# Performance work log

Hardware: AMD Instinct MI355X
Metric: run time of the kernel (lower is better)

Reference implementation:

```python
import jax, jax.numpy as jnp
import numpy as np
import math

N, LQ, DIM = 4, 1000, 256
HEADS, DHEAD, DEPTH = 8, 32, 2
LVLS, NPTS, MLP = 5, 4, 512
SCALE = DHEAD ** -0.5
SHAPES = np.array([[128, 128], [64, 64], [32, 32], [16, 16], [8, 8]], np.int32)
AREAS = SHAPES[:, 0] * SHAPES[:, 1]
STARTS = np.concatenate([[0], np.cumsum(AREAS)[:-1]]).astype(np.int32)
LIN = int(AREAS.sum())


def _ln(x, g, b):
    m = jnp.mean(x, -1, keepdims=True)
    v = jnp.var(x, -1, keepdims=True)
    return (x - m) * jax.lax.rsqrt(v + 1e-5) * g + b


def _gelu(x):  # tanh-approx GELU exactly as the torch module
    c = math.sqrt(2.0 / math.pi)
    return 0.5 * x * (1.0 + jnp.tanh(c * (x + 0.044715 * x ** 3)))


def _ms_deform(value, shapes, starts, loc, aw):
    # value [N,Lin,H,D]; loc [N,Lq,H,L,P,2] normalized to [0,1]; aw [N,Lq,H,L,P]
    n, lq, h, L, p, _ = loc.shape
    d = value.shape[-1]
    ni = jnp.arange(n)[:, None, None, None]
    hi = jnp.arange(h)[None, None, :, None]
    out = jnp.zeros((n, lq, h, d), value.dtype)
    for l in range(L):  # fixed small pyramid depth
        Hl, Wl = int(shapes[l, 0]), int(shapes[l, 1])
        s = int(starts[l])
        v = value[:, s:s + Hl * Wl].reshape(n, Hl, Wl, h, d)
        gx = loc[:, :, :, l, :, 0] * Wl - 0.5  # [N,Lq,H,P]
        gy = loc[:, :, :, l, :, 1] * Hl - 0.5
        x0 = jnp.floor(gx); y0 = jnp.floor(gy)
        lx = gx - x0; ly = gy - y0
        x0i = x0.astype(jnp.int32); y0i = y0.astype(jnp.int32)
        def corner(yi, xi):
            ok = ((yi >= 0) & (yi < Hl) & (xi >= 0) & (xi < Wl)).astype(value.dtype)
            g = v[ni, jnp.clip(yi, 0, Hl - 1), jnp.clip(xi, 0, Wl - 1), hi]  # [N,Lq,H,P,D]
            return g * ok[..., None]
        samp = (corner(y0i, x0i) * ((1 - ly) * (1 - lx))[..., None]
                + corner(y0i, x0i + 1) * ((1 - ly) * lx)[..., None]
                + corner(y0i + 1, x0i) * (ly * (1 - lx))[..., None]
                + corner(y0i + 1, x0i + 1) * (ly * lx)[..., None])
        out = out + jnp.einsum('nqhp,nqhpd->nqhd', aw[:, :, :, l], samp)
    return out.reshape(n, lq, h * d)


def _forward(x, src, center_pos, pos_w, pos_b, ln1_g, ln1_b, qkv_w, out_w, out_b,
             ln2_g, ln2_b, off_w, off_b, aw_w, aw_b, val_w, val_b, op_w, op_b,
             ln3_g, ln3_b, ff_w1, ff_b1, ff_w2, ff_b2, spatial_shapes, level_start_index):
    shapes = np.asarray(spatial_shapes)
    starts = np.asarray(level_start_index)
    n, lq, dim = x.shape
    pe = center_pos @ pos_w + pos_b                                   # pos_embedding(center_pos)
    ref = jnp.broadcast_to(center_pos[:, :, None, :], (n, lq, LVLS, 2))
    onorm = jnp.asarray(np.stack([shapes[:, 1], shapes[:, 0]], -1), x.dtype)  # [L,2] = (W,H)
    for i in range(DEPTH):
        # --- self-attention: PreNorm(x + pe) ---
        xn = _ln(x + pe, ln1_g[i], ln1_b[i])
        qkv = xn @ qkv_w[i]
        q, k, v = jnp.split(qkv, 3, axis=-1)
        q = q.reshape(n, lq, HEADS, DHEAD).transpose(0, 2, 1, 3)
        k = k.reshape(n, lq, HEADS, DHEAD).transpose(0, 2, 1, 3)
        v = v.reshape(n, lq, HEADS, DHEAD).transpose(0, 2, 1, 3)
        att = jax.nn.softmax(jnp.einsum('nhid,nhjd->nhij', q, k) * SCALE, axis=-1)
        o = jnp.einsum('nhij,nhjd->nhid', att, v).transpose(0, 2, 1, 3).reshape(n, lq, HEADS * DHEAD)
        x = x + o @ out_w[i] + out_b[i]
        # --- deformable cross-attention: PreNorm_CA norms query and src with same LN ---
        xn = _ln(x, ln2_g[i], ln2_b[i])
        srcn = _ln(src, ln2_g[i], ln2_b[i])
        query = xn + pe
        value = (srcn @ val_w[i] + val_b[i]).reshape(n, -1, HEADS, DHEAD)
        off = (query @ off_w[i] + off_b[i]).reshape(n, lq, HEADS, LVLS, NPTS, 2)
        aw = jax.nn.softmax((query @ aw_w[i] + aw_b[i]).reshape(n, lq, HEADS, LVLS * NPTS), axis=-1)
        aw = aw.reshape(n, lq, HEADS, LVLS, NPTS)
        loc = ref[:, :, None, :, None, :] + off / onorm[None, None, None, :, None, :]
        o = _ms_deform(value, shapes, starts, loc, aw)
        x = x + o @ op_w[i] + op_b[i]
        # --- feedforward: PreNorm ---
        xn = _ln(x, ln3_g[i], ln3_b[i])
        x = x + _gelu(xn @ ff_w1[i] + ff_b1[i]) @ ff_w2[i] + ff_b2[i]
    return x


def setup_inputs() -> dict:
    key = jax.random.key(0)
    ks = iter(jax.random.split(key, 64))
    r = lambda sh, s=0.02: jax.random.normal(next(ks), sh, jnp.float32) * s
    # sampling_offsets bias grid init (as in MSDeformAttn._reset_parameters)
    thetas = np.arange(HEADS) * (2.0 * math.pi / HEADS)
    grid = np.stack([np.cos(thetas), np.sin(thetas)], -1)
    grid = grid / np.abs(grid).max(-1, keepdims=True)
    grid = np.tile(grid[:, None, None, :], (1, LVLS, NPTS, 1)) * (np.arange(NPTS) + 1)[None, None, :, None]
    off_b = jnp.tile(jnp.asarray(grid.reshape(-1), jnp.float32)[None], (DEPTH, 1))
    return dict(
        x=jax.random.normal(next(ks), (N, LQ, DIM), jnp.float32),
        src=jax.random.normal(next(ks), (N, LIN, DIM), jnp.float32),
        center_pos=jax.random.uniform(next(ks), (N, LQ, 2), jnp.float32),
        spatial_shapes=jnp.asarray(SHAPES),
        level_start_index=jnp.asarray(STARTS),
        pos_w=r((2, DIM), 0.5), pos_b=jnp.zeros((DIM,), jnp.float32),
        ln1_g=jnp.ones((DEPTH, DIM), jnp.float32), ln1_b=jnp.zeros((DEPTH, DIM), jnp.float32),
        qkv_w=r((DEPTH, DIM, 3 * HEADS * DHEAD)),
        out_w=r((DEPTH, HEADS * DHEAD, DIM)), out_b=jnp.zeros((DEPTH, DIM), jnp.float32),
        ln2_g=jnp.ones((DEPTH, DIM), jnp.float32), ln2_b=jnp.zeros((DEPTH, DIM), jnp.float32),
        off_w=r((DEPTH, DIM, HEADS * LVLS * NPTS * 2)), off_b=off_b,
        aw_w=r((DEPTH, DIM, HEADS * LVLS * NPTS)), aw_b=jnp.zeros((DEPTH, HEADS * LVLS * NPTS), jnp.float32),
        val_w=r((DEPTH, DIM, HEADS * DHEAD)), val_b=jnp.zeros((DEPTH, HEADS * DHEAD), jnp.float32),
        op_w=r((DEPTH, HEADS * DHEAD, DIM)), op_b=jnp.zeros((DEPTH, DIM), jnp.float32),
        ln3_g=jnp.ones((DEPTH, DIM), jnp.float32), ln3_b=jnp.zeros((DEPTH, DIM), jnp.float32),
        ff_w1=r((DEPTH, DIM, MLP)), ff_b1=jnp.zeros((DEPTH, MLP), jnp.float32),
        ff_w2=r((DEPTH, MLP, DIM)), ff_b2=jnp.zeros((DEPTH, DIM), jnp.float32),
    )


def reference(x, src, center_pos, spatial_shapes, level_start_index, pos_w, pos_b,
              ln1_g, ln1_b, qkv_w, out_w, out_b, ln2_g, ln2_b, off_w, off_b,
              aw_w, aw_b, val_w, val_b, op_w, op_b, ln3_g, ln3_b,
              ff_w1, ff_b1, ff_w2, ff_b2):
    return _forward(x, src, center_pos, pos_w, pos_b, ln1_g, ln1_b, qkv_w, out_w, out_b,
                    ln2_g, ln2_b, off_w, off_b, aw_w, aw_b, val_w, val_b, op_w, op_b,
                    ln3_g, ln3_b, ff_w1, ff_b1, ff_w2, ff_b2, spatial_shapes, level_start_index)
```

## Files before the change

kernel.cpp:

```cpp
#include <hip/hip_runtime.h>
#include <hip/hip_bf16.h>
#include <math.h>

#define DIM 256
#define NB 4
#define LQ 1000
#define MLPD 512
#define LIN 21824
#define ROWS_X 4000
#define ROWS_SRC 87296
#define ATT_SCALE 0.17677669529663687f
#define LDK 72
#define VLAYER ((size_t)ROWS_SRC*256)

typedef __hip_bfloat16 bf16;
typedef __attribute__((ext_vector_type(8))) short short8;
typedef __attribute__((ext_vector_type(4))) float floatx4;

__device__ __forceinline__ float rdv(const void* p, int f, size_t i){
    if (f) return ((const float*)p)[i];
    unsigned u = ((unsigned)((const unsigned short*)p)[i]) << 16;
    union { unsigned u; float f; } c; c.u = u; return c.f;
}
__device__ __forceinline__ short f2bs(float v){
    bf16 h = __float2bfloat16(v);
    return *reinterpret_cast<short*>(&h);
}
__device__ __forceinline__ float bs2f(short s){
    union { unsigned u; float f; } c; c.u = ((unsigned)(unsigned short)s) << 16; return c.f;
}

__global__ void detect_kernel(const void* __restrict__ x, int* __restrict__ flag){
    const unsigned short* u = (const unsigned short*)x;
    int t = threadIdx.x;
    bool hit = false;
    #pragma unroll
    for (int k = 0; k < 4; ++k) {
        unsigned short b = u[(t*4 + k)*2];
        union { unsigned u; float f; } c; c.u = ((unsigned)b) << 16;
        if (!(fabsf(c.f) <= 1000.f)) hit = true;
    }
    unsigned long long m = __ballot(hit);
    __shared__ unsigned long long red[4];
    if ((t & 63) == 0) red[t >> 6] = m;
    __syncthreads();
    if (t == 0) flag[0] = ((red[0]|red[1]|red[2]|red[3]) != 0ULL) ? 1 : 0;
}

struct SetupTab {
    const void* csrc[13]; float* cdst[13];
    const void* cp; float* cpf;
    float* statz;
    const void* offb; const void* awb; float* oab;
    const void* src; bf16* srcn;
    const void* x; const void* posw; const void* posb;
    float* xf; float2* st; bf16* xab; float* pe;
    const void* wsrc[8]; short* wdst[8]; const void* wscl[8];
    const void* bfW[3]; const void* bfBv[3]; const void* bfBase[3]; float* bfDst[3];
};
__global__ __launch_bounds__(256) void setup_kernel(SetupTab t, const int* __restrict__ flag){
    int f = flag[0];
    int bid = blockIdx.x;
    int tid = threadIdx.x;
    __shared__ float tt[32][33];
    if (bid < 10912) {
        int half = tid >> 5, l = tid & 31;
        int row = bid*8 + half;
        float v[8];
        if (f) {
            const float4* p = (const float4*)((const float*)t.src + (size_t)row*DIM + l*8);
            float4 a = p[0], b = p[1];
            v[0]=a.x; v[1]=a.y; v[2]=a.z; v[3]=a.w;
            v[4]=b.x; v[5]=b.y; v[6]=b.z; v[7]=b.w;
        } else {
            short8 u = *(const short8*)((const short*)t.src + (size_t)row*DIM + l*8);
            #pragma unroll
            for (int j = 0; j < 8; ++j) v[j] = bs2f(u[j]);
        }
        float s = 0.f, s2 = 0.f;
        #pragma unroll
        for (int j = 0; j < 8; ++j) { s += v[j]; s2 += v[j]*v[j]; }
        #pragma unroll
        for (int o = 16; o; o >>= 1) {
            s  += __shfl_xor(s,  o, 32);
            s2 += __shfl_xor(s2, o, 32);
        }
        float mean = s * (1.f/DIM);
        float rstd = rsqrtf(s2 * (1.f/DIM) - mean*mean + 1e-5f);
        short8 o8;
        #pragma unroll
        for (int j = 0; j < 8; ++j) o8[j] = f2bs((v[j]-mean)*rstd);
        *(short8*)((short*)t.srcn + (size_t)row*DIM + l*8) = o8;
        return;
    }
    bid -= 10912;
    if (bid < 1520) {
        const int cum[9] = {0,192,256,336,376,440,504,632,760};
        const int wN[8]  = {768,256,320,160,256,256,512,256};
        const int wK[8]  = {256,256,256,256,256,256,256,512};
        const int wld[8] = {768,256,480,480,256,256,512,256};
        const int wro[8] = {0,0,0,320,0,0,0,0};
        int b = bid >= 760;
        int r = b ? bid - 760 : bid;
        int j = 0;
        #pragma unroll 1
        while (r >= cum[j+1]) ++j;
        int rel = r - cum[j];
        int ncols = wN[j] >> 5;
        int k0 = (rel / ncols) * 32, n0 = (rel % ncols) * 32;
        int K = wK[j], N = wN[j];
        int tx = tid & 31, ty = tid >> 5;
        size_t base = (size_t)b * K * N;
        for (int i = ty; i < 32; i += 8)
            tt[i][tx] = rdv(t.wsrc[j], f, base + (size_t)(k0+i)*N + (n0+tx));
        __syncthreads();
        int ld = wld[j], ro = wro[j];
        const void* sc = t.wscl[j];
        for (int i = ty; i < 32; i += 8) {
            int n = n0 + i, k = k0 + tx;
            float v = tt[tx][i];
            if (sc) v *= rdv(sc, f, (size_t)b*K + k);
            t.wdst[j][(size_t)b*ld*K + (size_t)(ro+n)*K + k] = f2bs(v);
        }
        return;
    }
    bid -= 1520;
    if (bid < 3072) {
        int b = bid >= 1536;
        int x = b ? bid - 1536 : bid;
        const int bN[3] = {768,512,256};
        int j, n;
        if (x < 768)       { j = 0; n = x; }
        else if (x < 1280) { j = 1; n = x - 768; }
        else               { j = 2; n = x - 1280; }
        int N = bN[j];
        int k = tid;
        float part = rdv(t.bfBv[j], f, (size_t)b*256 + k) *
                     rdv(t.bfW[j], f, (size_t)b*256*N + (size_t)k*N + n);
        #pragma unroll
        for (int o = 32; o; o >>= 1) part += __shfl_xor(part, o, 64);
        __shared__ float red[4];
        int wave = k >> 6, lane = k & 63;
        if (lane == 0) red[wave] = part;
        __syncthreads();
        if (k == 0) {
            float s = red[0] + red[1] + red[2] + red[3];
            if (t.bfBase[j]) s += rdv(t.bfBase[j], f, (size_t)b*N + n);
            t.bfDst[j][(size_t)b*N + n] = s;
        }
        return;
    }
    bid -= 3072;
    if (bid < 1000) {
        int wave = tid >> 6, lane = tid & 63;
        int row = bid*4 + wave;
        int c = lane*4;
        float4 v;
        if (f) v = *(const float4*)((const float*)t.x + (size_t)row*DIM + c);
        else {
            ushort4 u = *(const ushort4*)((const unsigned short*)t.x + (size_t)row*DIM + c);
            v = make_float4(bs2f((short)u.x), bs2f((short)u.y), bs2f((short)u.z), bs2f((short)u.w));
        }
        *(float4*)(t.xf + (size_t)row*DIM + c) = v;
        float cx = rdv(t.cp, f, (size_t)row*2), cy = rdv(t.cp, f, (size_t)row*2 + 1);
        float4 p;
        p.x = cx*rdv(t.posw, f, c)   + cy*rdv(t.posw, f, DIM+c)   + rdv(t.posb, f, c);
        p.y = cx*rdv(t.posw, f, c+1) + cy*rdv(t.posw, f, DIM+c+1) + rdv(t.posb, f, c+1);
        p.z = cx*rdv(t.posw, f, c+2) + cy*rdv(t.posw, f, DIM+c+2) + rdv(t.posb, f, c+2);
        p.w = cx*rdv(t.posw, f, c+3) + cy*rdv(t.posw, f, DIM+c+3) + rdv(t.posb, f, c+3);
        *(float4*)(t.pe + (size_t)row*DIM + c) = p;
        float a0 = v.x+p.x, a1 = v.y+p.y, a2 = v.z+p.z, a3 = v.w+p.w;
        float s  = a0+a1+a2+a3;
        float s2 = a0*a0+a1*a1+a2*a2+a3*a3;
        #pragma unroll
        for (int o = 32; o; o >>= 1) {
            s  += __shfl_xor(s,  o, 64);
            s2 += __shfl_xor(s2, o, 64);
        }
        if (lane == 0) t.st[row] = make_float2(s, s2);
        float mean = s * (1.f/DIM);
        float rstd = rsqrtf(s2 * (1.f/DIM) - mean*mean + 1e-5f);
        ushort4 o4;
        o4.x = (unsigned short)f2bs((a0-mean)*rstd);
        o4.y = (unsigned short)f2bs((a1-mean)*rstd);
        o4.z = (unsigned short)f2bs((a2-mean)*rstd);
        o4.w = (unsigned short)f2bs((a3-mean)*rstd);
        *(ushort4*)((unsigned short*)t.xab + (size_t)row*DIM + c) = o4;
        return;
    }
    bid -= 1000;
    if (bid < 27) {
        const int cs[14] = {0,2,3,5,7,9,11,13,15,17,19,21,25,27};
        const int ssz[13] = {512,256,512,512,512,512,512,512,512,512,512,1024,512};
        int j = 0;
        #pragma unroll 1
        while (bid >= cs[j+1]) ++j;
        int i = (bid - cs[j])*256 + tid;
        if (i < ssz[j]) t.cdst[j][i] = rdv(t.csrc[j], f, i);
        return;
    }
    bid -= 27;
    if (bid < 32) {
        int i = bid*256 + tid;
        if (i < ROWS_X*2) t.cpf[i] = rdv(t.cp, f, i);
        return;
    }
    bid -= 32;
    if (bid < 157) {
        int i = bid*256 + tid;
        if (i < 5*ROWS_X*2) t.statz[i] = 0.f;
        return;
    }
    bid -= 157;
    {
        int i = bid*256 + tid;
        if (i >= 960) return;
        int layer = i / 480, idx = i - layer*480;
        float v = (idx < 320) ? rdv(t.offb, f, (size_t)layer*320 + idx)
                              : rdv(t.awb,  f, (size_t)layer*160 + idx - 320);
        t.oab[i] = v;
    }
}

__global__ __launch_bounds__(256) void xnorm_kernel(const float* __restrict__ a,
        const float* __restrict__ pre, const float* __restrict__ post,
        const float2* __restrict__ sums, const float* __restrict__ g,
        const float* __restrict__ b, bf16* __restrict__ out){
    int wave = threadIdx.x >> 6, lane = threadIdx.x & 63;
    int row = blockIdx.x*4 + wave;
    float4 x = *(const float4*)(a + (size_t)row*DIM + lane*4);
    if (pre) {
        float4 p = *(const float4*)(pre + (size_t)row*DIM + lane*4);
        x.x += p.x; x.y += p.y; x.z += p.z; x.w += p.w;
    }
    float2 st = sums[row];
    float mean = st.x * (1.f/256.f);
    float rstd = rsqrtf(st.y*(1.f/256.f) - mean*mean + 1e-5f);
    float v0 = (x.x-mean)*rstd, v1 = (x.y-mean)*rstd;
    float v2 = (x.z-mean)*rstd, v3 = (x.w-mean)*rstd;
    if (g) {
        int c = lane*4;
        float4 gv = *(const float4*)(g + c);
        float4 bv = *(const float4*)(b + c);
        v0 = v0*gv.x + bv.x; v1 = v1*gv.y + bv.y;
        v2 = v2*gv.z + bv.z; v3 = v3*gv.w + bv.w;
    }
    if (post) {
        float4 p = *(const float4*)(post + (size_t)row*DIM + lane*4);
        v0 += p.x; v1 += p.y; v2 += p.z; v3 += p.w;
    }
    ushort4 o4;
    o4.x = (unsigned short)f2bs(v0); o4.y = (unsigned short)f2bs(v1);
    o4.z = (unsigned short)f2bs(v2); o4.w = (unsigned short)f2bs(v3);
    *(ushort4*)((unsigned short*)out + (size_t)row*DIM + lane*4) = o4;
}

__global__ __launch_bounds__(256) void mgemm_kernel(
    const short* __restrict__ A, const short* __restrict__ Wt,
    const float* __restrict__ bias, const float* __restrict__ res,
    void* __restrict__ Cout, int M, int K, int N, int act, int cbf,
    float2* __restrict__ statacc, const float* __restrict__ sepe,
    void* __restrict__ fin, const int* __restrict__ flag){
    __shared__ short As[64*LDK];
    __shared__ short Bs[64*LDK];
    int tid = threadIdx.x;
    int wave = tid >> 6, lane = tid & 63;
    int wm = wave >> 1, wn = wave & 1;
    int quad = lane >> 4, l16 = lane & 15;
    int row0 = blockIdx.x*64, col0 = blockIdx.y*64;
    floatx4 acc[2][2];
    #pragma unroll
    for (int i = 0; i < 2; ++i)
        #pragma unroll
        for (int j = 0; j < 2; ++j)
            acc[i][j] = (floatx4){0.f,0.f,0.f,0.f};

    int r  = tid >> 2;
    int kc = (tid & 3) * 16;
    int gr = row0 + r;
    int gc = col0 + r;
    const short8 z8 = {0,0,0,0,0,0,0,0};

    short8 ra0, ra1, rb0, rb1;
    if (gr < M) {
        const short8* p = (const short8*)(A + (size_t)gr*K + kc);
        ra0 = p[0]; ra1 = p[1];
    }
    if (gc < N) {
        const short8* p = (const short8*)(Wt + (size_t)gc*K + kc);
        rb0 = p[0]; rb1 = p[1];
    }

    for (int k0 = 0; k0 < K; k0 += 64) {
        short8 a0 = z8, a1 = z8;
        if (gr < M) { a0 = ra0; a1 = ra1; }
        *(short8*)&As[r*LDK + kc]     = a0;
        *(short8*)&As[r*LDK + kc + 8] = a1;
        short8 b0 = z8, b1 = z8;
        if (gc < N) { b0 = rb0; b1 = rb1; }
        *(short8*)&Bs[r*LDK + kc]     = b0;
        *(short8*)&Bs[r*LDK + kc + 8] = b1;
        int kn = k0 + 64;
        if (kn < K) {
            if (gr < M) {
                const short8* p = (const short8*)(A + (size_t)gr*K + kn + kc);
                ra0 = p[0]; ra1 = p[1];
            }
            if (gc < N) {
                const short8* p = (const short8*)(Wt + (size_t)gc*K + kn + kc);
                rb0 = p[0]; rb1 = p[1];
            }
        }
        __syncthreads();
        #pragma unroll
        for (int kb = 0; kb < 64; kb += 32) {
            short8 af[2], bfr[2];
            #pragma unroll
            for (int mi = 0; mi < 2; ++mi)
                af[mi] = *(const short8*)&As[(wm*32 + mi*16 + l16)*LDK + kb + quad*8];
            #pragma unroll
            for (int ni = 0; ni < 2; ++ni)
                bfr[ni] = *(const short8*)&Bs[(wn*32 + ni*16 + l16)*LDK + kb + quad*8];
            #pragma unroll
            for (int mi = 0; mi < 2; ++mi)
                #pragma unroll
                for (int ni = 0; ni < 2; ++ni)
                    acc[mi][ni] = __builtin_amdgcn_mfma_f32_16x16x32_bf16(
                        af[mi], bfr[ni], acc[mi][ni], 0, 0, 0);
        }
        __syncthreads();
    }
    float vout[2][2][4];
    #pragma unroll
    for (int mi = 0; mi < 2; ++mi) {
        int rbase = row0 + wm*32 + mi*16 + quad*4;
        #pragma unroll
        for (int ni = 0; ni < 2; ++ni) {
            int c = col0 + wn*32 + ni*16 + l16;
            #pragma unroll
            for (int r2 = 0; r2 < 4; ++r2) {
                int rr = rbase + r2;
                float v = 0.f;
                if (c < N && rr < M) {
                    v = acc[mi][ni][r2];
                    if (bias) v += bias[c];
                    if (act) {
                        float z = fminf(1.5957691216057308f*(v + 0.044715f*v*v*v), 60.f);
                        float e = __expf(z);
                        v = v * e / (e + 1.f);
                    }
                    if (res) v += res[(size_t)rr*N + c];
                }
                vout[mi][ni][r2] = v;
            }
        }
    }
    int fflag = 0;
    if (fin) fflag = flag[0];
    #pragma unroll
    for (int mi = 0; mi < 2; ++mi) {
        int rbase = row0 + wm*32 + mi*16 + quad*4;
        #pragma unroll
        for (int ni = 0; ni < 2; ++ni) {
            int c = col0 + wn*32 + ni*16 + l16;
            if (c >= N) continue;
            #pragma unroll
            for (int r2 = 0; r2 < 4; ++r2) {
                int rr = rbase + r2;
                if (rr >= M) continue;
                float v = vout[mi][ni][r2];
                if (fin) {
                    float w = isfinite(v) ? v : 0.f;
                    if (fflag) ((float*)fin)[(size_t)rr*N + c] = w;
                    else       ((bf16*)fin)[(size_t)rr*N + c] = __float2bfloat16(w);
                } else if (cbf) ((bf16*)Cout)[(size_t)rr*N + c] = __float2bfloat16(v);
                else            ((float*)Cout)[(size_t)rr*N + c] = v;
            }
        }
    }
    if (statacc) {
        #pragma unroll
        for (int mi = 0; mi < 2; ++mi) {
            int rbase = row0 + wm*32 + mi*16 + quad*4;
            #pragma unroll
            for (int r2 = 0; r2 < 4; ++r2) {
                int rr = rbase + r2;
                float sv = 0.f, sq = 0.f;
                #pragma unroll
                for (int ni = 0; ni < 2; ++ni) {
                    int c = col0 + wn*32 + ni*16 + l16;
                    float v = vout[mi][ni][r2];
                    if (sepe && rr < M) v += sepe[(size_t)rr*256 + c];
                    sv += v; sq += v*v;
                }
                #pragma unroll
                for (int o = 1; o < 16; o <<= 1) {
                    sv += __shfl_xor(sv, o, 64);
                    sq += __shfl_xor(sq, o, 64);
                }
                if (l16 == 0 && rr < M) {
                    atomicAdd(&statacc[rr].x, sv);
                    atomicAdd(&statacc[rr].y, sq);
                }
            }
        }
    }
}

__global__ __launch_bounds__(256) void mgemm128_kernel(
    const short* __restrict__ A, const short* __restrict__ Wt,
    const float* __restrict__ bias, bf16* __restrict__ valall){
    const int K = 256;
    __shared__ short lds[2*128*LDK];
    short* As = lds;
    short* Bs = lds + 128*LDK;
    int tid = threadIdx.x;
    int wave = tid >> 6, lane = tid & 63;
    int wm = wave >> 1, wn = wave & 1;
    int quad = lane >> 4, l16 = lane & 15;
    int bid = blockIdx.x;
    int panel, col;
    if (bid < 2720) {
        int g = bid >> 5, w = bid & 31;
        panel = g*8 + (w & 7);
        col = w >> 3;
    } else {
        int idx = bid - 2720;
        panel = 680 + (idx >> 2);
        col = idx & 3;
    }
    int row0 = panel*128, col0 = col*128;
    floatx4 acc[4][4];
    #pragma unroll
    for (int i = 0; i < 4; ++i)
        #pragma unroll
        for (int j = 0; j < 4; ++j)
            acc[i][j] = (floatx4){0.f,0.f,0.f,0.f};

    short8 pa[2][2], pb2[2][2];
    #pragma unroll
    for (int i = 0; i < 2; ++i) {
        int idx = tid + i*256;
        int rr = idx >> 2, kk = (idx & 3)*16;
        const short8* p = (const short8*)(A + (size_t)(row0+rr)*K + kk);
        pa[i][0] = p[0]; pa[i][1] = p[1];
        const short8* pb = (const short8*)(Wt + (size_t)(col0+rr)*K + kk);
        pb2[i][0] = pb[0]; pb2[i][1] = pb[1];
    }
    for (int k0 = 0; k0 < K; k0 += 64) {
        #pragma unroll
        for (int i = 0; i < 2; ++i) {
            int idx = tid + i*256;
            int rr = idx >> 2, kk = (idx & 3)*16;
            *(short8*)&As[rr*LDK + kk]     = pa[i][0];
            *(short8*)&As[rr*LDK + kk + 8] = pa[i][1];
            *(short8*)&Bs[rr*LDK + kk]     = pb2[i][0];
            *(short8*)&Bs[rr*LDK + kk + 8] = pb2[i][1];
        }
        int kn = k0 + 64;
        if (kn < K) {
            #pragma unroll
            for (int i = 0; i < 2; ++i) {
                int idx = tid + i*256;
                int rr = idx >> 2, kk = (idx & 3)*16;
                const short8* p = (const short8*)(A + (size_t)(row0+rr)*K + kn + kk);
                pa[i][0] = p[0]; pa[i][1] = p[1];
                const short8* pb = (const short8*)(Wt + (size_t)(col0+rr)*K + kn + kk);
                pb2[i][0] = pb[0]; pb2[i][1] = pb[1];
            }
        }
        __syncthreads();
        #pragma unroll
        for (int kb = 0; kb < 64; kb += 32) {
            short8 af[4], bfr[4];
            #pragma unroll
            for (int mi = 0; mi < 4; ++mi)
                af[mi] = *(const short8*)&As[(wm*64 + mi*16 + l16)*LDK + kb + quad*8];
            #pragma unroll
            for (int ni = 0; ni < 4; ++ni)
                bfr[ni] = *(const short8*)&Bs[(wn*64 + ni*16 + l16)*LDK + kb + quad*8];
            #pragma unroll
            for (int mi = 0; mi < 4; ++mi)
                #pragma unroll
                for (int ni = 0; ni < 4; ++ni)
                    acc[mi][ni] = __builtin_amdgcn_mfma_f32_16x16x32_bf16(
                        af[mi], bfr[ni], acc[mi][ni], 0, 0, 0);
        }
        __syncthreads();
    }
    short* Cs = lds;
    #pragma unroll
    for (int mi = 0; mi < 4; ++mi) {
        int lr = wm*64 + mi*16 + quad*4;
        #pragma unroll
        for (int ni = 0; ni < 4; ++ni) {
            int lc = wn*64 + ni*16 + l16;
            float bv = bias[col0 + lc];
            #pragma unroll
            for (int r2 = 0; r2 < 4; ++r2)
                Cs[(lr + r2)*136 + lc] = f2bs(acc[mi][ni][r2] + bv);
        }
    }
    __syncthreads();
    #pragma unroll
    for (int g = 0; g < 4; ++g) {
        int cbase = col0 + g*32;
        int l = cbase >> 8, h = (cbase & 255) >> 5;
        #pragma unroll
        for (int p = 0; p < 2; ++p) {
            int idx = p*256 + tid;
            int rr2 = idx >> 2;
            int dc = (idx & 3) * 8;
            short8 v = *(const short8*)&Cs[rr2*136 + g*32 + dc];
            int grr = row0 + rr2;
            unsigned n = (unsigned)grr / (unsigned)LIN;
            int pos = grr - (int)n*LIN;
            *(short8*)((short*)valall + (size_t)l*VLAYER
                       + ((size_t)(n*8+h)*LIN + pos)*32 + dc) = v;
        }
    }
}

__global__ __launch_bounds__(256) void fattn_kernel(const short* __restrict__ qkv,
                                                    bf16* __restrict__ out){
    int nh = blockIdx.y;
    int n = nh >> 3, h = nh & 7;
    int q0 = blockIdx.x * 64;
    __shared__ short Ks[64*40];
    __shared__ short VsT[32*72];
    __shared__ short Ps[64*72];
    int tid = threadIdx.x;
    int wave = tid >> 6, lane = tid & 63;
    int quad = lane >> 4, l16 = lane & 15;
    int r = tid >> 2, c8 = (tid & 3) * 8;
    const short8 z8 = {0,0,0,0,0,0,0,0};

    short8 qf = z8;
    {
        int gq = q0 + wave*16 + l16;
        if (gq < LQ) {
            short8 s = *(const short8*)(qkv + ((size_t)(n*LQ+gq))*768 + h*32 + quad*8);
            #pragma unroll
            for (int j = 0; j < 8; ++j) qf[j] = f2bs(bs2f(s[j]) * ATT_SCALE);
        }
    }
    floatx4 acc[2];
    acc[0] = (floatx4){0.f,0.f,0.f,0.f};
    acc[1] = (floatx4){0.f,0.f,0.f,0.f};
    float m[4], lsum[4];
    #pragma unroll
    for (int i = 0; i < 4; ++i) { m[i] = -3.0e38f; lsum[i] = 0.f; }

    short8 kvp = z8, vvp = z8;
    if (r < LQ) {
        const short* rp = qkv + ((size_t)(n*LQ+r))*768;
        kvp = *(const short8*)(rp + 256 + h*32 + c8);
        vvp = *(const short8*)(rp + 512 + h*32 + c8);
    }
    for (int k0 = 0; k0 < LQ; k0 += 64) {
        *(short8*)&Ks[r*40 + c8] = kvp;
        #pragma unroll
        for (int j = 0; j < 8; ++j) VsT[(c8+j)*72 + r] = vvp[j];
        short8 kvn = z8, vvn = z8;
        if (k0 + 64 < LQ) {
            int gk = k0 + 64 + r;
            if (gk < LQ) {
                const short* rp = qkv + ((size_t)(n*LQ+gk))*768;
                kvn = *(const short8*)(rp + 256 + h*32 + c8);
                vvn = *(const short8*)(rp + 512 + h*32 + c8);
            }
        }
        __syncthreads();
        floatx4 s4[4];
        #pragma unroll
        for (int kg = 0; kg < 4; ++kg) {
            short8 bfr = *(const short8*)&Ks[(kg*16 + l16)*40 + quad*8];
            s4[kg] = __builtin_amdgcn_mfma_f32_16x16x32_bf16(
                qf, bfr, (floatx4){0.f,0.f,0.f,0.f}, 0, 0, 0);
        }
        if (k0 + 64 > LQ) {
            #pragma unroll
            for (int kg = 0; kg < 4; ++kg)
                if (k0 + kg*16 + l16 >= LQ)
                    s4[kg] = (floatx4){-3.0e38f,-3.0e38f,-3.0e38f,-3.0e38f};
        }
        float fac[4], psum[4];
        #pragma unroll
        for (int r2 = 0; r2 < 4; ++r2) {
            float v = fmaxf(fmaxf(s4[0][r2], s4[1][r2]), fmaxf(s4[2][r2], s4[3][r2]));
            v = fmaxf(v, __shfl_xor(v, 1, 64));
            v = fmaxf(v, __shfl_xor(v, 2, 64));
            v = fmaxf(v, __shfl_xor(v, 4, 64));
            v = fmaxf(v, __shfl_xor(v, 8, 64));
            float mn = fmaxf(m[r2], v);
            fac[r2] = __expf(m[r2] - mn);
            m[r2] = mn;
            psum[r2] = 0.f;
        }
        #pragma unroll
        for (int kg = 0; kg < 4; ++kg)
            #pragma unroll
            for (int r2 = 0; r2 < 4; ++r2) {
                float pv = __expf(s4[kg][r2] - m[r2]);
                psum[r2] += pv;
                Ps[(wave*16 + quad*4 + r2)*72 + kg*16 + l16] = f2bs(pv);
            }
        #pragma unroll
        for (int r2 = 0; r2 < 4; ++r2) {
            psum[r2] += __shfl_xor(psum[r2], 1, 64);
            psum[r2] += __shfl_xor(psum[r2], 2, 64);
            psum[r2] += __shfl_xor(psum[r2], 4, 64);
            psum[r2] += __shfl_xor(psum[r2], 8, 64);
            lsum[r2] = lsum[r2]*fac[r2] + psum[r2];
        }
        #pragma unroll
        for (int ni = 0; ni < 2; ++ni)
            #pragma unroll
            for (int r2 = 0; r2 < 4; ++r2)
                acc[ni][r2] *= fac[r2];
        #pragma unroll
        for (int kb = 0; kb < 64; kb += 32) {
            short8 pf = *(const short8*)&Ps[(wave*16 + l16)*72 + kb + quad*8];
            #pragma unroll
            for (int ni = 0; ni < 2; ++ni) {
                short8 vf = *(const short8*)&VsT[(ni*16 + l16)*72 + kb + quad*8];
                acc[ni] = __builtin_amdgcn_mfma_f32_16x16x32_bf16(pf, vf, acc[ni], 0, 0, 0);
            }
        }
        __syncthreads();
        kvp = kvn; vvp = vvn;
    }
    #pragma unroll
    for (int r2 = 0; r2 < 4; ++r2) {
        int row = q0 + wave*16 + quad*4 + r2;
        if (row >= LQ) continue;
        float inv = 1.f / lsum[r2];
        #pragma unroll
        for (int ni = 0; ni < 2; ++ni)
            out[((size_t)(n*LQ+row))*256 + h*32 + ni*16 + l16] =
                __float2bfloat16(acc[ni][r2] * inv);
    }
}

__global__ __launch_bounds__(256) void sample2_kernel(
        const bf16* __restrict__ value, const float* __restrict__ offaw,
        const float* __restrict__ cp, bf16* __restrict__ out){
    int nq = blockIdx.x;
    int n = nq / LQ;
    int d = threadIdx.x & 31, h = threadIdx.x >> 5;
    float cx = cp[nq*2], cy = cp[nq*2+1];
    const float* rowp = offaw + (size_t)nq*480;
    float o0 = rowp[h*40 + d];
    float o1 = (d < 8) ? rowp[h*40 + 32 + d] : 0.f;
    float logit = (d < 20) ? rowp[320 + h*20 + d] : -3.0e38f;
    float mx = logit;
    #pragma unroll
    for (int off = 16; off; off >>= 1) mx = fmaxf(mx, __shfl_xor(mx, off, 32));
    float p = (d < 20) ? __expf(logit - mx) : 0.f;
    float sm = p;
    #pragma unroll
    for (int off = 16; off; off >>= 1) sm += __shfl_xor(sm, off, 32);
    p *= (1.f / sm);

    const int HW[5] = {128,64,32,16,8};
    const int ST[5] = {0,16384,20480,21504,21760};
    float acc = 0.f;
    #pragma unroll
    for (int l = 0; l < 5; ++l) {
        int hw = HW[l];
        float fhw = (float)hw;
        size_t vb = ((size_t)(n*8 + h)*LIN + ST[l])*32 + d;
        #pragma unroll
        for (int pi = 0; pi < 4; ++pi) {
            const int idx = l*4 + pi;
            float w  = __shfl(p, idx, 32);
            float ox = (2*idx < 32)   ? __shfl(o0, 2*idx, 32)   : __shfl(o1, 2*idx-32, 32);
            float oy = (2*idx+1 < 32) ? __shfl(o0, 2*idx+1, 32) : __shfl(o1, 2*idx+1-32, 32);
            float gx = cx*fhw + ox - 0.5f;
            float gy = cy*fhw + oy - 0.5f;
            float x0f = floorf(gx), y0f = floorf(gy);
            float lx = gx - x0f, ly = gy - y0f;
            int x0 = (int)x0f, y0 = (int)y0f;
            int x1 = x0 + 1, y1 = y0 + 1;
            bool bx0 = (unsigned)x0 < (unsigned)hw, bx1 = (unsigned)x1 < (unsigned)hw;
            bool by0 = (unsigned)y0 < (unsigned)hw, by1 = (unsigned)y1 < (unsigned)hw;
            int x0c = min(max(x0, 0), hw-1), x1c = min(max(x1, 0), hw-1);
            int y0c = min(max(y0, 0), hw-1), y1c = min(max(y1, 0), hw-1);
            float v00 = __bfloat162float(value[vb + (size_t)(y0c*hw + x0c)*32]);
            float v01 = __bfloat162float(value[vb + (size_t)(y0c*hw + x1c)*32]);
            float v10 = __bfloat162float(value[vb + (size_t)(y1c*hw + x0c)*32]);
            float v11 = __bfloat162float(value[vb + (size_t)(y1c*hw + x1c)*32]);
            float w00 = (bx0 && by0) ? (1.f-ly)*(1.f-lx)*w : 0.f;
            float w01 = (bx1 && by0) ? (1.f-ly)*lx*w       : 0.f;
            float w10 = (bx0 && by1) ? ly*(1.f-lx)*w       : 0.f;
            float w11 = (bx1 && by1) ? ly*lx*w             : 0.f;
            acc = fmaf(w00, v00, acc);
            acc = fmaf(w01, v01, acc);
            acc = fmaf(w10, v10, acc);
            acc = fmaf(w11, v11, acc);
        }
    }
    out[(size_t)nq*256 + h*32 + d] = __float2bfloat16(acc);
}

extern "C" void kernel_launch(void* const* d_in, const int* in_sizes, int n_in,
                              void* d_out, int out_size, void* d_ws, size_t ws_size,
                              hipStream_t stream){
    const void* x_raw  = d_in[0];
    const void* src    = d_in[1];
    const void* cp_raw = d_in[2];
    char* ws = (char*)d_ws;
    size_t off = 0;
    auto alloc = [&](size_t bytes){ size_t p = off; off += (bytes + 255) & ~(size_t)255; return p; };
    int*   flag  = (int*)(ws + alloc(256));
    float* xf    = (float*)(ws + alloc((size_t)ROWS_X*DIM*4));
    float* pe    = (float*)(ws + alloc((size_t)ROWS_X*DIM*4));
    bf16*  tmpb  = (bf16*)(ws + alloc((size_t)ROWS_X*DIM*2));
    bf16*  xab   = (bf16*)(ws + alloc((size_t)ROWS_X*DIM*2));
    bf16*  qkv   = (bf16*)(ws + alloc((size_t)ROWS_X*768*2));
    bf16*  ffh   = (bf16*)(ws + alloc((size_t)ROWS_X*MLPD*2));
    float* offaw = (float*)(ws + alloc((size_t)ROWS_X*480*4));
    float* cpf   = (float*)(ws + alloc((size_t)ROWS_X*2*4));
    float* oab   = (float*)(ws + alloc((size_t)2*480*4));
    float2* statbuf = (float2*)(ws + alloc((size_t)6*ROWS_X*8));
    float* qkvB  = (float*)(ws + alloc((size_t)2*768*4));
    float* ff1B  = (float*)(ws + alloc((size_t)2*512*4));
    float* valB  = (float*)(ws + alloc((size_t)2*256*4));
    const int sidx[13] = {5,6,7,8,11,12,13,19,21,22,23,25,27};
    const int ssz[13]  = {512,256,512,512,512,512,512,512,512,512,512,1024,512};
    float* sp[13];
    for (int j = 0; j < 13; ++j) sp[j] = (float*)(ws + alloc((size_t)ssz[j]*4));
    short* qkvT = (short*)(ws + alloc((size_t)2*768*256*2));
    short* outT = (short*)(ws + alloc((size_t)2*256*256*2));
    short* oawT = (short*)(ws + alloc((size_t)2*480*256*2));
    short* valT = (short*)(ws + alloc((size_t)2*256*256*2));
    short* opT  = (short*)(ws + alloc((size_t)2*256*256*2));
    short* ff1T = (short*)(ws + alloc((size_t)2*512*256*2));
    short* ff2T = (short*)(ws + alloc((size_t)2*256*512*2));
    bf16*  srcn = (bf16*)(ws + alloc((size_t)ROWS_SRC*DIM*2));
    bf16*  valall = (bf16*)(ws + alloc((size_t)2*ROWS_SRC*DIM*2));
    (void)ws_size; (void)in_sizes; (void)n_in; (void)out_size;

    float* ln2_g = sp[5];  float* ln2_b = sp[6];
    float* out_b = sp[4];
    float* op_b  = sp[8];
    float* ff_b2 = sp[12];

    detect_kernel<<<1, 256, 0, stream>>>(x_raw, flag);
    {
        SetupTab t;
        for (int j = 0; j < 13; ++j) { t.csrc[j] = d_in[sidx[j]]; t.cdst[j] = sp[j]; }
        t.cp = cp_raw; t.cpf = cpf;
        t.statz = (float*)(statbuf + ROWS_X);
        t.offb = d_in[15]; t.awb = d_in[17]; t.oab = oab;
        t.src = src; t.srcn = srcn;
        t.x = x_raw; t.posw = d_in[5]; t.posb = d_in[6];
        t.xf = xf; t.st = statbuf; t.xab = xab; t.pe = pe;
        const int widx[8] = {9,10,14,16,18,20,24,26};
        short* wdst[8] = {qkvT, outT, oawT, oawT, valT, opT, ff1T, ff2T};
        const void* wscl[8] = {d_in[7], nullptr, nullptr, nullptr, d_in[12], nullptr, d_in[22], nullptr};
        for (int j = 0; j < 8; ++j) { t.wsrc[j] = d_in[widx[j]]; t.wdst[j] = wdst[j]; t.wscl[j] = wscl[j]; }
        t.bfW[0] = d_in[9];  t.bfBv[0] = d_in[8];  t.bfBase[0] = nullptr;  t.bfDst[0] = qkvB;
        t.bfW[1] = d_in[24]; t.bfBv[1] = d_in[23]; t.bfBase[1] = d_in[25]; t.bfDst[1] = ff1B;
        t.bfW[2] = d_in[18]; t.bfBv[2] = d_in[13]; t.bfBase[2] = d_in[19]; t.bfDst[2] = valB;
        setup_kernel<<<16724, 256, 0, stream>>>(t, flag);
    }
    mgemm128_kernel<<<(ROWS_SRC/128)*4, 256, 0, stream>>>(
        (const short*)srcn, valT, valB, valall);

    int gmx = (ROWS_X + 63) / 64;
    for (int i = 0; i < 2; ++i) {
        float2* stA = statbuf + (size_t)(i ? 3 : 0)*ROWS_X;
        float2* stO = statbuf + (size_t)(i ? 4 : 1)*ROWS_X;
        float2* stF = statbuf + (size_t)(i ? 5 : 2)*ROWS_X;
        if (i == 1)
            xnorm_kernel<<<ROWS_X/4, 256, 0, stream>>>(xf, pe, nullptr, stA,
                                                       nullptr, nullptr, xab);
        mgemm_kernel<<<dim3(gmx,12), 256, 0, stream>>>(
            (const short*)xab, qkvT + (size_t)i*768*256, qkvB + i*768, nullptr, qkv,
            ROWS_X, 256, 768, 0, 1, nullptr, nullptr, nullptr, flag);
        fattn_kernel<<<dim3(16,32), 256, 0, stream>>>((const short*)qkv, tmpb);
        mgemm_kernel<<<dim3(gmx,4), 256, 0, stream>>>(
            (const short*)tmpb, outT + (size_t)i*256*256, out_b + i*DIM, xf, xf,
            ROWS_X, 256, 256, 0, 0, stO, nullptr, nullptr, flag);
        xnorm_kernel<<<ROWS_X/4, 256, 0, stream>>>(xf, nullptr, pe, stO,
                                                   ln2_g + i*DIM, ln2_b + i*DIM, xab);
        mgemm_kernel<<<dim3(gmx,8), 256, 0, stream>>>(
            (const short*)xab, oawT + (size_t)i*480*256, oab + i*480, nullptr, offaw,
            ROWS_X, 256, 480, 0, 0, nullptr, nullptr, nullptr, flag);
        sample2_kernel<<<ROWS_X, 256, 0, stream>>>(
            valall + (size_t)i*VLAYER, offaw, cpf, tmpb);
        mgemm_kernel<<<dim3(gmx,4), 256, 0, stream>>>(
            (const short*)tmpb, opT + (size_t)i*256*256, op_b + i*DIM, xf, xf,
            ROWS_X, 256, 256, 0, 0, stF, nullptr, nullptr, flag);
        xnorm_kernel<<<ROWS_X/4, 256, 0, stream>>>(xf, nullptr, nullptr, stF,
                                                   nullptr, nullptr, xab);
        mgemm_kernel<<<dim3(gmx,8), 256, 0, stream>>>(
            (const short*)xab, ff1T + (size_t)i*512*256, ff1B + i*MLPD, nullptr, ffh,
            ROWS_X, 256, 512, 1, 1, nullptr, nullptr, nullptr, flag);
        if (i == 0) {
            mgemm_kernel<<<dim3(gmx,4), 256, 0, stream>>>(
                (const short*)ffh, ff2T + (size_t)i*256*512, ff_b2 + i*DIM, xf, xf,
                ROWS_X, 512, 256, 0, 0, statbuf + (size_t)3*ROWS_X, pe, nullptr, flag);
        } else {
            mgemm_kernel<<<dim3(gmx,4), 256, 0, stream>>>(
                (const short*)ffh, ff2T + (size_t)i*256*512, ff_b2 + i*DIM, xf, xf,
                ROWS_X, 512, 256, 0, 0, nullptr, nullptr, d_out, flag);
        }
    }
}
```

Before: 543.1 us.

## Fuse source LayerNorm into value-projection GEMM A-tile load

```diff
diff --git a/kernel.cpp b/kernel.cpp
--- a/kernel.cpp
+++ b/kernel.cpp
@@ -52,7 +52,6 @@
     const void* cp; float* cpf;
     float* statz;
     const void* offb; const void* awb; float* oab;
-    const void* src; bf16* srcn;
     const void* x; const void* posw; const void* posb;
     float* xf; float2* st; bf16* xab; float* pe;
     const void* wsrc[8]; short* wdst[8]; const void* wscl[8];
@@ -63,37 +62,6 @@
     int bid = blockIdx.x;
     int tid = threadIdx.x;
     __shared__ float tt[32][33];
-    if (bid < 10912) {
-        int half = tid >> 5, l = tid & 31;
-        int row = bid*8 + half;
-        float v[8];
-        if (f) {
-            const float4* p = (const float4*)((const float*)t.src + (size_t)row*DIM + l*8);
-            float4 a = p[0], b = p[1];
-            v[0]=a.x; v[1]=a.y; v[2]=a.z; v[3]=a.w;
-            v[4]=b.x; v[5]=b.y; v[6]=b.z; v[7]=b.w;
-        } else {
-            short8 u = *(const short8*)((const short*)t.src + (size_t)row*DIM + l*8);
-            #pragma unroll
-            for (int j = 0; j < 8; ++j) v[j] = bs2f(u[j]);
-        }
-        float s = 0.f, s2 = 0.f;
-        #pragma unroll
-        for (int j = 0; j < 8; ++j) { s += v[j]; s2 += v[j]*v[j]; }
-        #pragma unroll
-        for (int o = 16; o; o >>= 1) {
-            s  += __shfl_xor(s,  o, 32);
-            s2 += __shfl_xor(s2, o, 32);
-        }
-        float mean = s * (1.f/DIM);
-        float rstd = rsqrtf(s2 * (1.f/DIM) - mean*mean + 1e-5f);
-        short8 o8;
-        #pragma unroll
-        for (int j = 0; j < 8; ++j) o8[j] = f2bs((v[j]-mean)*rstd);
-        *(short8*)((short*)t.srcn + (size_t)row*DIM + l*8) = o8;
-        return;
-    }
-    bid -= 10912;
     if (bid < 1520) {
         const int cum[9] = {0,192,256,336,376,440,504,632,760};
         const int wN[8]  = {768,256,320,160,256,256,512,256};
@@ -408,13 +376,15 @@
 }
 
 __global__ __launch_bounds__(256) void mgemm128_kernel(
-    const short* __restrict__ A, const short* __restrict__ Wt,
-    const float* __restrict__ bias, bf16* __restrict__ valall){
+    const void* __restrict__ src, const int* __restrict__ flag,
+    const short* __restrict__ Wt, const float* __restrict__ bias,
+    bf16* __restrict__ valall){
     const int K = 256;
     __shared__ short lds[2*128*LDK];
     short* As = lds;
     short* Bs = lds + 128*LDK;
     int tid = threadIdx.x;
+    int f = flag[0];
     int wave = tid >> 6, lane = tid & 63;
     int wm = wave >> 1, wn = wave & 1;
     int quad = lane >> 4, l16 = lane & 15;
@@ -430,6 +400,37 @@
         col = idx & 3;
     }
     int row0 = panel*128, col0 = col*128;
+    int rq = tid >> 2;
+    int kc = (tid & 3) * 16;
+    float mean[2], rstd[2];
+    #pragma unroll
+    for (int i = 0; i < 2; ++i) {
+        size_t base = (size_t)(row0 + i*64 + rq)*K + kc;
+        float s = 0.f, q = 0.f;
+        #pragma unroll
+        for (int k0 = 0; k0 < K; k0 += 64) {
+            if (f) {
+                const float4* p = (const float4*)((const float*)src + base + k0);
+                float4 a = p[0], b = p[1], c = p[2], d = p[3];
+                s += a.x+a.y+a.z+a.w + b.x+b.y+b.z+b.w
+                   + c.x+c.y+c.z+c.w + d.x+d.y+d.z+d.w;
+                q += a.x*a.x+a.y*a.y+a.z*a.z+a.w*a.w + b.x*b.x+b.y*b.y+b.z*b.z+b.w*b.w
+                   + c.x*c.x+c.y*c.y+c.z*c.z+c.w*c.w + d.x*d.x+d.y*d.y+d.z*d.z+d.w*d.w;
+            } else {
+                const short8* p = (const short8*)((const short*)src + base + k0);
+                short8 u0 = p[0], u1 = p[1];
+                #pragma unroll
+                for (int j = 0; j < 8; ++j) {
+                    float v0 = bs2f(u0[j]), v1 = bs2f(u1[j]);
+                    s += v0 + v1; q += v0*v0 + v1*v1;
+                }
+            }
+        }
+        s += __shfl_xor(s, 1, 64); s += __shfl_xor(s, 2, 64);
+        q += __shfl_xor(q, 1, 64); q += __shfl_xor(q, 2, 64);
+        mean[i] = s * (1.f/256.f);
+        rstd[i] = rsqrtf(q*(1.f/256.f) - mean[i]*mean[i] + 1e-5f);
+    }
     floatx4 acc[4][4];
     #pragma unroll
     for (int i = 0; i < 4; ++i)
@@ -437,35 +438,47 @@
         for (int j = 0; j < 4; ++j)
             acc[i][j] = (floatx4){0.f,0.f,0.f,0.f};
 
-    short8 pa[2][2], pb2[2][2];
+    short8 pb2[2][2];
     #pragma unroll
     for (int i = 0; i < 2; ++i) {
-        int idx = tid + i*256;
-        int rr = idx >> 2, kk = (idx & 3)*16;
-        const short8* p = (const short8*)(A + (size_t)(row0+rr)*K + kk);
-        pa[i][0] = p[0]; pa[i][1] = p[1];
-        const short8* pb = (const short8*)(Wt + (size_t)(col0+rr)*K + kk);
+        const short8* pb = (const short8*)(Wt + (size_t)(col0 + i*64 + rq)*K + kc);
         pb2[i][0] = pb[0]; pb2[i][1] = pb[1];
     }
     for (int k0 = 0; k0 < K; k0 += 64) {
         #pragma unroll
         for (int i = 0; i < 2; ++i) {
-            int idx = tid + i*256;
-            int rr = idx >> 2, kk = (idx & 3)*16;
-            *(short8*)&As[rr*LDK + kk]     = pa[i][0];
-            *(short8*)&As[rr*LDK + kk + 8] = pa[i][1];
-            *(short8*)&Bs[rr*LDK + kk]     = pb2[i][0];
-            *(short8*)&Bs[rr*LDK + kk + 8] = pb2[i][1];
+            int rr = i*64 + rq;
+            size_t abase = (size_t)(row0 + rr)*K + k0 + kc;
+            short8 a0, a1;
+            if (f) {
+                const float4* p = (const float4*)((const float*)src + abase);
+                float4 x0 = p[0], x1 = p[1], x2 = p[2], x3 = p[3];
+                float av[16] = {x0.x,x0.y,x0.z,x0.w, x1.x,x1.y,x1.z,x1.w,
+                                x2.x,x2.y,x2.z,x2.w, x3.x,x3.y,x3.z,x3.w};
+                #pragma unroll
+                for (int j = 0; j < 8; ++j) {
+                    a0[j] = f2bs((av[j]   - mean[i])*rstd[i]);
+                    a1[j] = f2bs((av[8+j] - mean[i])*rstd[i]);
+                }
+            } else {
+                const short8* p = (const short8*)((const short*)src + abase);
+                short8 u0 = p[0], u1 = p[1];
+                #pragma unroll
+                for (int j = 0; j < 8; ++j) {
+                    a0[j] = f2bs((bs2f(u0[j]) - mean[i])*rstd[i]);
+                    a1[j] = f2bs((bs2f(u1[j]) - mean[i])*rstd[i]);
+                }
+            }
+            *(short8*)&As[rr*LDK + kc]     = a0;
+            *(short8*)&As[rr*LDK + kc + 8] = a1;
+            *(short8*)&Bs[rr*LDK + kc]     = pb2[i][0];
+            *(short8*)&Bs[rr*LDK + kc + 8] = pb2[i][1];
         }
         int kn = k0 + 64;
         if (kn < K) {
             #pragma unroll
             for (int i = 0; i < 2; ++i) {
-                int idx = tid + i*256;
-                int rr = idx >> 2, kk = (idx & 3)*16;
-                const short8* p = (const short8*)(A + (size_t)(row0+rr)*K + kn + kk);
-                pa[i][0] = p[0]; pa[i][1] = p[1];
-                const short8* pb = (const short8*)(Wt + (size_t)(col0+rr)*K + kn + kk);
+                const short8* pb = (const short8*)(Wt + (size_t)(col0 + i*64 + rq)*K + kn + kc);
                 pb2[i][0] = pb[0]; pb2[i][1] = pb[1];
             }
         }
@@ -737,7 +750,6 @@
     short* opT  = (short*)(ws + alloc((size_t)2*256*256*2));
     short* ff1T = (short*)(ws + alloc((size_t)2*512*256*2));
     short* ff2T = (short*)(ws + alloc((size_t)2*256*512*2));
-    bf16*  srcn = (bf16*)(ws + alloc((size_t)ROWS_SRC*DIM*2));
     bf16*  valall = (bf16*)(ws + alloc((size_t)2*ROWS_SRC*DIM*2));
     (void)ws_size; (void)in_sizes; (void)n_in; (void)out_size;
 
@@ -753,7 +765,6 @@
         t.cp = cp_raw; t.cpf = cpf;
         t.statz = (float*)(statbuf + ROWS_X);
         t.offb = d_in[15]; t.awb = d_in[17]; t.oab = oab;
-        t.src = src; t.srcn = srcn;
         t.x = x_raw; t.posw = d_in[5]; t.posb = d_in[6];
         t.xf = xf; t.st = statbuf; t.xab = xab; t.pe = pe;
         const int widx[8] = {9,10,14,16,18,20,24,26};
@@ -763,10 +774,10 @@
         t.bfW[0] = d_in[9];  t.bfBv[0] = d_in[8];  t.bfBase[0] = nullptr;  t.bfDst[0] = qkvB;
         t.bfW[1] = d_in[24]; t.bfBv[1] = d_in[23]; t.bfBase[1] = d_in[25]; t.bfDst[1] = ff1B;
         t.bfW[2] = d_in[18]; t.bfBv[2] = d_in[13]; t.bfBase[2] = d_in[19]; t.bfDst[2] = valB;
-        setup_kernel<<<16724, 256, 0, stream>>>(t, flag);
+        setup_kernel<<<5812, 256, 0, stream>>>(t, flag);
     }
     mgemm128_kernel<<<(ROWS_SRC/128)*4, 256, 0, stream>>>(
-        (const short*)srcn, valT, valB, valall);
+        src, flag, valT, valB, valall);
 
     int gmx = (ROWS_X + 63) / 64;
     for (int i = 0; i < 2; ++i) {
```

Measured after the change: 574.3 us. +5.7%, slower.
